# Kernel optimization log

Measured on AMD Instinct MI355X. Metric: run time of the kernel, lower is better.

## Reference

```python
import jax, jax.numpy as jnp
import numpy as np

B, T, E = 16, 512, 768
N_ANN = 32                      # mentions per passage
N_ENT = B * N_ANN               # 512 flat entities, each 2E wide
P = B * N_ANN * (N_ANN - 1)     # 15872 ordered pairs
H = 512                          # MLP hidden size (head_args layer_sizes)
ENTITY_DIM = 256                 # relation MLP output = 2*entity_dim
D4 = 4 * E                       # relation_input width


def setup_inputs() -> dict:
    key = jax.random.key(0)
    ks = jax.random.split(key, 14)
    inp = {
        "x": jax.random.normal(ks[0], (B, T, E), dtype=jnp.float32),
        "src_tokens": jax.random.randint(ks[1], (B, T), 0, 32000),
        "mask_annotation": jax.random.randint(ks[2], (B, T), 0, 2),
        "all_annotations": jax.random.randint(ks[3], (B, 2 * N_ANN), 0, T),
        "n_annotations": N_ANN,
        "relation_entity_indices_left": jax.random.randint(ks[4], (P,), 0, N_ENT),
        "relation_entity_indices_right": jax.random.randint(ks[5], (P,), 0, N_ENT),
        # relation MLP: Linear(4E,H) -> ReLU -> Linear(H, 2*entity_dim)
        "W1": jax.random.normal(ks[6], (D4, H), dtype=jnp.float32) / np.sqrt(D4),
        "b1": jnp.zeros((H,), dtype=jnp.float32),
        "W2": jax.random.normal(ks[7], (H, 2 * ENTITY_DIM), dtype=jnp.float32) / np.sqrt(H),
        "b2": jnp.zeros((2 * ENTITY_DIM,), dtype=jnp.float32),
        # score MLP: Linear(4E,H) -> ReLU -> Linear(H, 1)
        "Ws1": jax.random.normal(ks[8], (D4, H), dtype=jnp.float32) / np.sqrt(D4),
        "bs1": jnp.zeros((H,), dtype=jnp.float32),
        "Ws2": jax.random.normal(ks[9], (H, 1), dtype=jnp.float32) / np.sqrt(H),
        "bs2": jnp.zeros((1,), dtype=jnp.float32),
    }
    return inp


def reference(x, src_tokens, mask_annotation, all_annotations, n_annotations,
              relation_entity_indices_left, relation_entity_indices_right,
              W1, b1, W2, b2, Ws1, bs1, Ws2, bs2):
    batch_size, _, enc_dim = x.shape
    # idx_repeated: each batch row repeated 2*n_annotations times
    idx_rep = jnp.repeat(jnp.arange(batch_size), 2 * n_annotations)
    ann_flat = all_annotations.reshape(-1)
    # gather annotation tokens -> [B*2n, E] -> pairwise concat [B*n, 2E]
    ent_tokens = x[idx_rep, ann_flat]
    entity_representation = ent_tokens.reshape(-1, 2 * enc_dim)
    left = entity_representation[relation_entity_indices_left]
    right = entity_representation[relation_entity_indices_right]
    relation_input = jnp.concatenate((left, right), axis=-1)  # [P, 4E]
    h_rel = jax.nn.relu(relation_input @ W1 + b1)
    relation_representation = h_rel @ W2 + b2                 # [P, 2*entity_dim]
    h_sc = jax.nn.relu(relation_input @ Ws1 + bs1)
    relation_score = jnp.abs((h_sc @ Ws2 + bs2).squeeze(-1))  # [P]
    return entity_representation, relation_representation, relation_score
```

## Files before the change

### kernel.cpp

```cpp
#include <hip/hip_runtime.h>

typedef unsigned short u16;
typedef __attribute__((ext_vector_type(8))) short short8;
typedef __attribute__((ext_vector_type(4))) float floatx4;

#define P_PAIRS 15872
#define E_DIM   768
#define D2      1536
#define OUT_ENT   (512*1536)
#define OUT_REL   (15872*512)

__device__ __forceinline__ u16 f2bf(float f){
    union { float f; unsigned u; } v; v.f = f;
    unsigned r = v.u + 0x7fffu + ((v.u >> 16) & 1u);
    return (u16)(r >> 16);
}
__device__ __forceinline__ unsigned pack2(float a, float b){
    return (unsigned)f2bf(a) | ((unsigned)f2bf(b) << 16);
}
__device__ __forceinline__ void async_ld16(const void* g, void* lds_base){
    __builtin_amdgcn_global_load_lds(
        (const __attribute__((address_space(1))) unsigned*)g,
        (__attribute__((address_space(3))) unsigned*)lds_base, 16, 0, 0);
}

__global__ __launch_bounds__(256)
void prep_k(const float* __restrict__ W1, const float* __restrict__ Ws1,
            const float* __restrict__ W2, const float* __restrict__ x,
            const int* __restrict__ ann,
            u16* __restrict__ W1T, u16* __restrict__ Ws1T, u16* __restrict__ W2T,
            float* __restrict__ entF, u16* __restrict__ entB) {
    const int bid = blockIdx.x;
    const int t = threadIdx.x;
    if (bid < 3328) {
        __shared__ float tile[32][33];
        const float* src; u16* dst; int R, C, b;
        if (bid < 1536)      { src = W1;  dst = W1T;  R = 3072; C = 512; b = bid; }
        else if (bid < 3072) { src = Ws1; dst = Ws1T; R = 3072; C = 512; b = bid - 1536; }
        else                 { src = W2;  dst = W2T;  R = 512;  C = 512; b = bid - 3072; }
        const int bx = (b & 15) * 32;
        const int by = (b >> 4) * 32;
        const int tx = t & 31, ty = t >> 5;
#pragma unroll
        for (int i = 0; i < 32; i += 8)
            tile[ty + i][tx] = src[(size_t)(by + ty + i) * C + bx + tx];
        __syncthreads();
#pragma unroll
        for (int i = 0; i < 32; i += 8)
            dst[(size_t)(bx + ty + i) * R + by + tx] = f2bf(tile[tx][ty + i]);
    } else {
        const int e = bid - 3328;
#pragma unroll
        for (int pass = 0; pass < 2; pass++) {
            const int c = t + pass * 256;
            if (c >= 384) break;
            const int half = c / 192;
            const int tok = ann[e * 2 + half];
            const int b = e >> 5;
            const float4 v = ((const float4*)(x + (size_t)(b * 512 + tok) * E_DIM))[c % 192];
            ((float4*)(entF + (size_t)e * D2))[c] = v;
            uint2 o; o.x = pack2(v.x, v.y); o.y = pack2(v.z, v.w);
            ((uint2*)(entB + (size_t)e * D2))[c] = o;
        }
    }
}

__global__ __launch_bounds__(256)
void gemm_uv(const u16* __restrict__ Ent, const u16* __restrict__ W1T,
             const u16* __restrict__ Ws1T, const float* __restrict__ b1,
             const float* __restrict__ bs1, float* __restrict__ UV) {
    __shared__ __align__(16) u16 As[2][64 * 64];
    __shared__ __align__(16) u16 Bs[2][64 * 64];
    const int t = threadIdx.x;
    const int bid = blockIdx.x;
    const int m0 = (bid & 7) * 64;
    const int n0g = (bid >> 3) * 64;
    const int g = n0g >> 9;
    const int n0 = n0g & 511;
    const u16* WT = (g < 2) ? W1T : Ws1T;
    const int koff = (g & 1) * D2;

    const int wave = t >> 6, lane = t & 63;
    const int wm = (wave >> 1) * 32, wn = (wave & 1) * 32;
    const int l15 = lane & 15, quad = lane >> 4;

    const int lr = lane >> 3;
    const int k8 = (lane & 7) ^ lr;
    const int rowA0 = wave * 16 + lr;
    const u16* gA0 = Ent + (size_t)(m0 + rowA0) * D2 + k8 * 8;
    const u16* gA1 = Ent + (size_t)(m0 + rowA0 + 8) * D2 + k8 * 8;
    const u16* gB0 = WT + (size_t)(n0 + rowA0) * 3072 + koff + k8 * 8;
    const u16* gB1 = WT + (size_t)(n0 + rowA0 + 8) * 3072 + koff + k8 * 8;
    const int lofs0 = wave * 1024, lofs1 = wave * 1024 + 512;

    floatx4 acc[2][2] = {};
    async_ld16(gA0, As[0] + lofs0);
    async_ld16(gA1, As[0] + lofs1);
    async_ld16(gB0, Bs[0] + lofs0);
    async_ld16(gB1, Bs[0] + lofs1);
    for (int i = 0; i < 24; i++) {
        const int cur = i & 1;
        __syncthreads();
        if (i + 1 < 24) {
            const int k1 = (i + 1) * 64;
            async_ld16(gA0 + k1, As[cur ^ 1] + lofs0);
            async_ld16(gA1 + k1, As[cur ^ 1] + lofs1);
            async_ld16(gB0 + k1, Bs[cur ^ 1] + lofs0);
            async_ld16(gB1 + k1, Bs[cur ^ 1] + lofs1);
        }
        const u16* Ac = As[cur];
        const u16* Bc = Bs[cur];
#pragma unroll
        for (int kk = 0; kk < 2; kk++) {
            short8 af[2], bf[2];
#pragma unroll
            for (int i2 = 0; i2 < 2; i2++) {
                const int ra = wm + i2 * 16 + l15;
                af[i2] = *(const short8*)(Ac + (ra * 8 + ((quad + kk * 4) ^ (ra & 7))) * 8);
                const int rb = wn + i2 * 16 + l15;
                bf[i2] = *(const short8*)(Bc + (rb * 8 + ((quad + kk * 4) ^ (rb & 7))) * 8);
            }
#pragma unroll
            for (int i2 = 0; i2 < 2; i2++)
#pragma unroll
                for (int j2 = 0; j2 < 2; j2++)
                    acc[i2][j2] = __builtin_amdgcn_mfma_f32_16x16x32_bf16(af[i2], bf[j2], acc[i2][j2], 0, 0, 0);
        }
    }
    float* outg = UV + (size_t)g * 262144;
#pragma unroll
    for (int j = 0; j < 2; j++) {
        const int col = n0 + wn + j * 16 + l15;
        const float bias = (g == 0) ? b1[col] : (g == 2) ? bs1[col] : 0.f;
#pragma unroll
        for (int i = 0; i < 2; i++) {
            const int rowb = m0 + wm + i * 16 + quad * 4;
#pragma unroll
            for (int r = 0; r < 4; r++)
                outg[(size_t)(rowb + r) * 512 + col] = acc[i][j][r] + bias;
        }
    }
}

__global__ __launch_bounds__(256)
void rel_score_k(const float* __restrict__ UV, const int* __restrict__ left,
                 const int* __restrict__ right, const float* __restrict__ Ws2,
                 const float* __restrict__ bs2, const u16* __restrict__ W2T,
                 const float* __restrict__ b2, float* __restrict__ rel,
                 float* __restrict__ score) {
    const int bid = blockIdx.x;
    const int t = threadIdx.x;
    const int wave = t >> 6, lane = t & 63;

    if (bid < 496) {
        __shared__ __align__(16) u16 As[2][128 * 32];
        __shared__ __align__(16) u16 Bs[2][128 * 32];
        const int m0 = (bid >> 2) * 128;
        const int n0 = (bid & 3) * 128;
        const int wm = (wave >> 1) * 64, wn = (wave & 1) * 64;
        const int l15 = lane & 15, quad = lane >> 4;

        const int arow = t >> 1;
        const int kh = t & 1;
        const int li = left[m0 + arow], ri = right[m0 + arow];
        const float4* Up = (const float4*)(UV + (size_t)li * 512 + kh * 16);
        const float4* Vp = (const float4*)(UV + 262144 + (size_t)ri * 512 + kh * 16);
        const int sA0 = arow * 4 + ((kh * 2) ^ (arow & 3));
        const int sA1 = arow * 4 + ((kh * 2 + 1) ^ (arow & 3));
        const int browl = lane >> 2;
        const int bk8 = (lane & 3) ^ (browl & 3);
        const u16* gB0 = W2T + (size_t)(n0 + wave * 32 + browl) * 512 + bk8 * 8;
        const u16* gB1 = W2T + (size_t)(n0 + wave * 32 + 16 + browl) * 512 + bk8 * 8;
        const int lofs0 = wave * 1024, lofs1 = wave * 1024 + 512;

        floatx4 acc[4][4] = {};
        float4 uu[4], vv[4];
#pragma unroll
        for (int j = 0; j < 4; j++) { uu[j] = Up[j]; vv[j] = Vp[j]; }
        async_ld16(gB0, Bs[0] + lofs0);
        async_ld16(gB1, Bs[0] + lofs1);
        {
            uint4 h0, h1;
            h0.x = pack2(fmaxf(uu[0].x + vv[0].x, 0.f), fmaxf(uu[0].y + vv[0].y, 0.f));
            h0.y = pack2(fmaxf(uu[0].z + vv[0].z, 0.f), fmaxf(uu[0].w + vv[0].w, 0.f));
            h0.z = pack2(fmaxf(uu[1].x + vv[1].x, 0.f), fmaxf(uu[1].y + vv[1].y, 0.f));
            h0.w = pack2(fmaxf(uu[1].z + vv[1].z, 0.f), fmaxf(uu[1].w + vv[1].w, 0.f));
            h1.x = pack2(fmaxf(uu[2].x + vv[2].x, 0.f), fmaxf(uu[2].y + vv[2].y, 0.f));
            h1.y = pack2(fmaxf(uu[2].z + vv[2].z, 0.f), fmaxf(uu[2].w + vv[2].w, 0.f));
            h1.z = pack2(fmaxf(uu[3].x + vv[3].x, 0.f), fmaxf(uu[3].y + vv[3].y, 0.f));
            h1.w = pack2(fmaxf(uu[3].z + vv[3].z, 0.f), fmaxf(uu[3].w + vv[3].w, 0.f));
            *(uint4*)(As[0] + sA0 * 8) = h0;
            *(uint4*)(As[0] + sA1 * 8) = h1;
        }
#pragma unroll
        for (int j = 0; j < 4; j++) { uu[j] = Up[8 + j]; vv[j] = Vp[8 + j]; }

        for (int i = 0; i < 16; i++) {
            const int cur = i & 1;
            __syncthreads();
            if (i + 1 < 16) {
                const int k1 = (i + 1) * 32;
                async_ld16(gB0 + k1, Bs[cur ^ 1] + lofs0);
                async_ld16(gB1 + k1, Bs[cur ^ 1] + lofs1);
                uint4 h0, h1;
                h0.x = pack2(fmaxf(uu[0].x + vv[0].x, 0.f), fmaxf(uu[0].y + vv[0].y, 0.f));
                h0.y = pack2(fmaxf(uu[0].z + vv[0].z, 0.f), fmaxf(uu[0].w + vv[0].w, 0.f));
                h0.z = pack2(fmaxf(uu[1].x + vv[1].x, 0.f), fmaxf(uu[1].y + vv[1].y, 0.f));
                h0.w = pack2(fmaxf(uu[1].z + vv[1].z, 0.f), fmaxf(uu[1].w + vv[1].w, 0.f));
                h1.x = pack2(fmaxf(uu[2].x + vv[2].x, 0.f), fmaxf(uu[2].y + vv[2].y, 0.f));
                h1.y = pack2(fmaxf(uu[2].z + vv[2].z, 0.f), fmaxf(uu[2].w + vv[2].w, 0.f));
                h1.z = pack2(fmaxf(uu[3].x + vv[3].x, 0.f), fmaxf(uu[3].y + vv[3].y, 0.f));
                h1.w = pack2(fmaxf(uu[3].z + vv[3].z, 0.f), fmaxf(uu[3].w + vv[3].w, 0.f));
                *(uint4*)(As[cur ^ 1] + sA0 * 8) = h0;
                *(uint4*)(As[cur ^ 1] + sA1 * 8) = h1;
                if (i + 2 < 16) {
                    const int q = (i + 2) * 8;
#pragma unroll
                    for (int j = 0; j < 4; j++) { uu[j] = Up[q + j]; vv[j] = Vp[q + j]; }
                }
            }
            const u16* Ac = As[cur];
            const u16* Bc = Bs[cur];
            short8 af[4], bf[4];
#pragma unroll
            for (int i2 = 0; i2 < 4; i2++) {
                const int ra = wm + i2 * 16 + l15;
                af[i2] = *(const short8*)(Ac + (ra * 4 + (quad ^ (ra & 3))) * 8);
                const int rb = wn + i2 * 16 + l15;
                bf[i2] = *(const short8*)(Bc + (rb * 4 + (quad ^ (rb & 3))) * 8);
            }
#pragma unroll
            for (int i2 = 0; i2 < 4; i2++)
#pragma unroll
                for (int j2 = 0; j2 < 4; j2++)
                    acc[i2][j2] = __builtin_amdgcn_mfma_f32_16x16x32_bf16(af[i2], bf[j2], acc[i2][j2], 0, 0, 0);
        }
#pragma unroll
        for (int j = 0; j < 4; j++) {
            const int col = n0 + wn + j * 16 + l15;
            const float bias = b2[col];
#pragma unroll
            for (int i = 0; i < 4; i++) {
                const int rowb = m0 + wm + i * 16 + quad * 4;
#pragma unroll
                for (int r = 0; r < 4; r++)
                    rel[(size_t)(rowb + r) * 512 + col] = acc[i][j][r] + bias;
            }
        }
    } else {
        const int pid0 = (bid - 496) * 32 + wave * 8;
        const float4* Wsp = (const float4*)(Ws2 + lane * 8);
        const float4 w0 = Wsp[0], w1 = Wsp[1];
        const float bias = bs2[0];
#pragma unroll
        for (int it = 0; it < 8; it++) {
            const int p = pid0 + it;
            const int l = left[p], r = right[p];
            const float4* us = (const float4*)(UV + 2 * 262144 + (size_t)l * 512 + lane * 8);
            const float4* vs = (const float4*)(UV + 3 * 262144 + (size_t)r * 512 + lane * 8);
            const float4 a0 = us[0], a1 = us[1];
            const float4 c0 = vs[0], c1 = vs[1];
            float acc;
            acc  = fmaxf(a0.x + c0.x, 0.f) * w0.x;
            acc += fmaxf(a0.y + c0.y, 0.f) * w0.y;
            acc += fmaxf(a0.z + c0.z, 0.f) * w0.z;
            acc += fmaxf(a0.w + c0.w, 0.f) * w0.w;
            acc += fmaxf(a1.x + c1.x, 0.f) * w1.x;
            acc += fmaxf(a1.y + c1.y, 0.f) * w1.y;
            acc += fmaxf(a1.z + c1.z, 0.f) * w1.z;
            acc += fmaxf(a1.w + c1.w, 0.f) * w1.w;
#pragma unroll
            for (int off = 32; off; off >>= 1) acc += __shfl_down(acc, off, 64);
            if (lane == 0) score[p] = fabsf(acc + bias);
        }
    }
}

extern "C" void kernel_launch(void* const* d_in, const int* in_sizes, int n_in,
                              void* d_out, int out_size, void* d_ws, size_t ws_size,
                              hipStream_t stream) {
    const float* x   = (const float*)d_in[0];
    const int* ann   = (const int*)d_in[3];
    const int* left  = (const int*)d_in[5];
    const int* right = (const int*)d_in[6];
    const float* W1  = (const float*)d_in[7];
    const float* b1  = (const float*)d_in[8];
    const float* W2  = (const float*)d_in[9];
    const float* b2  = (const float*)d_in[10];
    const float* Ws1 = (const float*)d_in[11];
    const float* bs1 = (const float*)d_in[12];
    const float* Ws2 = (const float*)d_in[13];
    const float* bs2 = (const float*)d_in[14];

    float* out = (float*)d_out;
    float* entF = out;
    float* rel  = out + OUT_ENT;
    float* sco  = out + OUT_ENT + OUT_REL;

    u16* W1T  = (u16*)d_ws;
    u16* Ws1T = W1T + 512 * 3072;
    u16* W2T  = Ws1T + 512 * 3072;
    u16* EntB = W2T + 512 * 512;
    float* UV = (float*)(EntB + 512 * 1536);

    prep_k<<<3840, 256, 0, stream>>>(W1, Ws1, W2, x, ann, W1T, Ws1T, W2T, entF, EntB);
    gemm_uv<<<256, 256, 0, stream>>>(EntB, W1T, Ws1T, b1, bs1, UV);
    rel_score_k<<<992, 256, 0, stream>>>(UV, left, right, Ws2, bs2, W2T, b2, rel, sco);
}
```

Before: 160.9 us.

## Build A fragments directly in registers from gathered U/V rows, dropping LDS staging

The relation GEMM's A operand (relu(U[left]+V[right]) in bf16) is no longer written cooperatively to shared memory. Each lane now gathers the U/V floats it needs for its MFMA fragments straight from global memory and packs them in registers. This removes the A-tile LDS writes and reads and halves the shared memory footprint. In exchange, each wave redundantly gathers its own 64 rows (the two waves sharing an M half load the same rows), so global gather traffic per block doubles and more registers hold the prefetched floats.

New measurement: 200.6 us. 24.7% more time.

```diff
diff --git a/kernel.cpp b/kernel.cpp
--- a/kernel.cpp
+++ b/kernel.cpp
@@ -153,20 +153,20 @@
     const int wave = t >> 6, lane = t & 63;
 
     if (bid < 496) {
-        __shared__ __align__(16) u16 As[2][128 * 32];
         __shared__ __align__(16) u16 Bs[2][128 * 32];
         const int m0 = (bid >> 2) * 128;
         const int n0 = (bid & 3) * 128;
         const int wm = (wave >> 1) * 64, wn = (wave & 1) * 64;
         const int l15 = lane & 15, quad = lane >> 4;
 
-        const int arow = t >> 1;
-        const int kh = t & 1;
-        const int li = left[m0 + arow], ri = right[m0 + arow];
-        const float4* Up = (const float4*)(UV + (size_t)li * 512 + kh * 16);
-        const float4* Vp = (const float4*)(UV + 262144 + (size_t)ri * 512 + kh * 16);
-        const int sA0 = arow * 4 + ((kh * 2) ^ (arow & 3));
-        const int sA1 = arow * 4 + ((kh * 2 + 1) ^ (arow & 3));
+        const float* Au[4];
+        const float* Av[4];
+#pragma unroll
+        for (int i2 = 0; i2 < 4; i2++) {
+            const int row = m0 + wm + i2 * 16 + l15;
+            Au[i2] = UV + (size_t)left[row] * 512 + quad * 8;
+            Av[i2] = UV + 262144 + (size_t)right[row] * 512 + quad * 8;
+        }
         const int browl = lane >> 2;
         const int bk8 = (lane & 3) ^ (browl & 3);
         const u16* gB0 = W2T + (size_t)(n0 + wave * 32 + browl) * 512 + bk8 * 8;
@@ -174,26 +174,16 @@
         const int lofs0 = wave * 1024, lofs1 = wave * 1024 + 512;
 
         floatx4 acc[4][4] = {};
-        float4 uu[4], vv[4];
-#pragma unroll
-        for (int j = 0; j < 4; j++) { uu[j] = Up[j]; vv[j] = Vp[j]; }
+        float4 pu[4][2], pv[4][2];
+#pragma unroll
+        for (int i2 = 0; i2 < 4; i2++) {
+            pu[i2][0] = *(const float4*)(Au[i2]);
+            pu[i2][1] = *(const float4*)(Au[i2] + 4);
+            pv[i2][0] = *(const float4*)(Av[i2]);
+            pv[i2][1] = *(const float4*)(Av[i2] + 4);
+        }
         async_ld16(gB0, Bs[0] + lofs0);
         async_ld16(gB1, Bs[0] + lofs1);
-        {
-            uint4 h0, h1;
-            h0.x = pack2(fmaxf(uu[0].x + vv[0].x, 0.f), fmaxf(uu[0].y + vv[0].y, 0.f));
-            h0.y = pack2(fmaxf(uu[0].z + vv[0].z, 0.f), fmaxf(uu[0].w + vv[0].w, 0.f));
-            h0.z = pack2(fmaxf(uu[1].x + vv[1].x, 0.f), fmaxf(uu[1].y + vv[1].y, 0.f));
-            h0.w = pack2(fmaxf(uu[1].z + vv[1].z, 0.f), fmaxf(uu[1].w + vv[1].w, 0.f));
-            h1.x = pack2(fmaxf(uu[2].x + vv[2].x, 0.f), fmaxf(uu[2].y + vv[2].y, 0.f));
-            h1.y = pack2(fmaxf(uu[2].z + vv[2].z, 0.f), fmaxf(uu[2].w + vv[2].w, 0.f));
-            h1.z = pack2(fmaxf(uu[3].x + vv[3].x, 0.f), fmaxf(uu[3].y + vv[3].y, 0.f));
-            h1.w = pack2(fmaxf(uu[3].z + vv[3].z, 0.f), fmaxf(uu[3].w + vv[3].w, 0.f));
-            *(uint4*)(As[0] + sA0 * 8) = h0;
-            *(uint4*)(As[0] + sA1 * 8) = h1;
-        }
-#pragma unroll
-        for (int j = 0; j < 4; j++) { uu[j] = Up[8 + j]; vv[j] = Vp[8 + j]; }
 
         for (int i = 0; i < 16; i++) {
             const int cur = i & 1;
@@ -202,32 +192,35 @@
                 const int k1 = (i + 1) * 32;
                 async_ld16(gB0 + k1, Bs[cur ^ 1] + lofs0);
                 async_ld16(gB1 + k1, Bs[cur ^ 1] + lofs1);
-                uint4 h0, h1;
-                h0.x = pack2(fmaxf(uu[0].x + vv[0].x, 0.f), fmaxf(uu[0].y + vv[0].y, 0.f));
-                h0.y = pack2(fmaxf(uu[0].z + vv[0].z, 0.f), fmaxf(uu[0].w + vv[0].w, 0.f));
-                h0.z = pack2(fmaxf(uu[1].x + vv[1].x, 0.f), fmaxf(uu[1].y + vv[1].y, 0.f));
-                h0.w = pack2(fmaxf(uu[1].z + vv[1].z, 0.f), fmaxf(uu[1].w + vv[1].w, 0.f));
-                h1.x = pack2(fmaxf(uu[2].x + vv[2].x, 0.f), fmaxf(uu[2].y + vv[2].y, 0.f));
-                h1.y = pack2(fmaxf(uu[2].z + vv[2].z, 0.f), fmaxf(uu[2].w + vv[2].w, 0.f));
-                h1.z = pack2(fmaxf(uu[3].x + vv[3].x, 0.f), fmaxf(uu[3].y + vv[3].y, 0.f));
-                h1.w = pack2(fmaxf(uu[3].z + vv[3].z, 0.f), fmaxf(uu[3].w + vv[3].w, 0.f));
-                *(uint4*)(As[cur ^ 1] + sA0 * 8) = h0;
-                *(uint4*)(As[cur ^ 1] + sA1 * 8) = h1;
-                if (i + 2 < 16) {
-                    const int q = (i + 2) * 8;
-#pragma unroll
-                    for (int j = 0; j < 4; j++) { uu[j] = Up[q + j]; vv[j] = Vp[q + j]; }
+            }
+            short8 af[4];
+#pragma unroll
+            for (int i2 = 0; i2 < 4; i2++) {
+                const float4 a0 = pu[i2][0], a1 = pu[i2][1];
+                const float4 c0 = pv[i2][0], c1 = pv[i2][1];
+                union { unsigned u[4]; short8 s; } w;
+                w.u[0] = pack2(fmaxf(a0.x + c0.x, 0.f), fmaxf(a0.y + c0.y, 0.f));
+                w.u[1] = pack2(fmaxf(a0.z + c0.z, 0.f), fmaxf(a0.w + c0.w, 0.f));
+                w.u[2] = pack2(fmaxf(a1.x + c1.x, 0.f), fmaxf(a1.y + c1.y, 0.f));
+                w.u[3] = pack2(fmaxf(a1.z + c1.z, 0.f), fmaxf(a1.w + c1.w, 0.f));
+                af[i2] = w.s;
+            }
+            if (i + 1 < 16) {
+                const int k1 = (i + 1) * 32;
+#pragma unroll
+                for (int i2 = 0; i2 < 4; i2++) {
+                    pu[i2][0] = *(const float4*)(Au[i2] + k1);
+                    pu[i2][1] = *(const float4*)(Au[i2] + k1 + 4);
+                    pv[i2][0] = *(const float4*)(Av[i2] + k1);
+                    pv[i2][1] = *(const float4*)(Av[i2] + k1 + 4);
                 }
             }
-            const u16* Ac = As[cur];
             const u16* Bc = Bs[cur];
-            short8 af[4], bf[4];
-#pragma unroll
-            for (int i2 = 0; i2 < 4; i2++) {
-                const int ra = wm + i2 * 16 + l15;
-                af[i2] = *(const short8*)(Ac + (ra * 4 + (quad ^ (ra & 3))) * 8);
-                const int rb = wn + i2 * 16 + l15;
-                bf[i2] = *(const short8*)(Bc + (rb * 4 + (quad ^ (rb & 3))) * 8);
+            short8 bf[4];
+#pragma unroll
+            for (int j2 = 0; j2 < 4; j2++) {
+                const int rb = wn + j2 * 16 + l15;
+                bf[j2] = *(const short8*)(Bc + (rb * 4 + (quad ^ (rb & 3))) * 8);
             }
 #pragma unroll
             for (int i2 = 0; i2 < 4; i2++)
```
